# Performance work log

Hardware: AMD Instinct MI355X
Metric: run time of the kernel (lower is better)

Reference implementation:

```python
import jax, jax.numpy as jnp
import numpy as np
from jax import lax

CHAR_EMB = 30      # char_embedding_dim
N_FILT = 30        # num_cnn_filter (depthwise multiplier)
KSIZE = 3          # char_kernel_size
WORD_EMB = 100     # word_embedding_dim
MAX_WLEN = 40      # max_word_len
N_CHARS = 102      # characters.id + 2
VOCAB = 400002     # GloVe 400k + unk + pad


def setup_inputs() -> dict:
    key = jax.random.key(0)
    k1, k2, k3, k4, k5, k6 = jax.random.split(key, 6)
    B, S = 64, 128
    char_ids = jax.random.randint(k1, (B, S, MAX_WLEN), 0, N_CHARS)
    word_ids = jax.random.randint(k2, (B, S), 0, VOCAB)
    bound = (3.0 / CHAR_EMB) ** 0.5
    char_emb = jax.random.uniform(k3, (N_CHARS, CHAR_EMB), minval=-bound, maxval=bound, dtype=jnp.float32)
    # grouped Conv1d: out=CHAR_EMB*N_FILT=900, in_per_group=1, kernel=3 (OIH layout)
    fan = 1 * KSIZE + N_FILT * KSIZE
    xav = (6.0 / fan) ** 0.5
    conv_w = jax.random.uniform(k4, (CHAR_EMB * N_FILT, 1, KSIZE), minval=-xav, maxval=xav, dtype=jnp.float32)
    conv_b = jnp.zeros((CHAR_EMB * N_FILT,), dtype=jnp.float32)
    glove = jax.random.normal(k5, (VOCAB, WORD_EMB), dtype=jnp.float32)
    return {"char_ids": char_ids, "word_ids": word_ids, "char_emb": char_emb,
            "conv_w": conv_w, "conv_b": conv_b, "glove": glove}


def reference(char_ids, word_ids, char_emb, conv_w, conv_b, glove):
    B, S, W = char_ids.shape
    # char embedding lookup: [B,S,W,E] -> NCH layout [B*S, E, W]
    x = char_emb[char_ids]                       # [B,S,W,30]
    x = jnp.transpose(x, (0, 1, 3, 2)).reshape(B * S, CHAR_EMB, W)
    # depthwise (grouped) conv, groups=30, multiplier=30 -> 900 out channels, length W-K+1
    y = lax.conv_general_dilated(
        x, conv_w, window_strides=(1,), padding="VALID",
        dimension_numbers=("NCH", "OIH", "NCH"),
        feature_group_count=CHAR_EMB)            # [B*S, 900, 38]
    y = y + conv_b[None, :, None]
    pooled = jnp.max(y, axis=2).reshape(B, S, CHAR_EMB * N_FILT)  # max-over-time
    glove_e = glove[word_ids]                    # [B,S,100]
    return jnp.concatenate([pooled, glove_e], axis=2)  # [B,S,1000]
```

## Files before the change

### kernel.cpp

```cpp
#include <hip/hip_runtime.h>
#include <hip/hip_bf16.h>

#define CHAR_EMB 30
#define NFILT    30
#define WLEN     40
#define TOUT     38
#define OUTC     900
#define WORD_EMB 100
#define ROWP     44

__global__ __launch_bounds__(256) void encoder_kernel(
    const int*   __restrict__ char_ids,
    const int*   __restrict__ word_ids,
    const float* __restrict__ char_emb,
    const float* __restrict__ conv_w,
    const float* __restrict__ conv_b,
    const float* __restrict__ glove,
    float*       __restrict__ out,
    int BS)
{
    const int n   = blockIdx.x;
    const int tid = threadIdx.x;

    __shared__ float xs[CHAR_EMB * ROWP];
    __shared__ int   cid[WLEN];

    if (tid < WLEN) cid[tid] = char_ids[n * WLEN + tid];
    __syncthreads();

    for (int i = tid; i < WLEN * CHAR_EMB; i += 256) {
        const int t = i / CHAR_EMB;
        const int c = i - t * CHAR_EMB;
        xs[c * ROWP + t] = char_emb[cid[t] * CHAR_EMB + c];
    }
    __syncthreads();

    float* orow = out + (long)n * (OUTC + WORD_EMB);

    for (int o = tid; o < OUTC; o += 256) {
        const int g = o / NFILT;
        const float w0 = conv_w[o * 3 + 0];
        const float w1 = conv_w[o * 3 + 1];
        const float w2 = conv_w[o * 3 + 2];

        float xr[WLEN];
        const float4* rp = reinterpret_cast<const float4*>(&xs[g * ROWP]);
        #pragma unroll
        for (int k = 0; k < WLEN / 4; ++k) {
            float4 q = rp[k];
            xr[4 * k + 0] = q.x;
            xr[4 * k + 1] = q.y;
            xr[4 * k + 2] = q.z;
            xr[4 * k + 3] = q.w;
        }

        float m = -3.4e38f;
        #pragma unroll
        for (int t = 0; t < TOUT; ++t) {
            float v = fmaf(w0, xr[t], fmaf(w1, xr[t + 1], w2 * xr[t + 2]));
            m = fmaxf(m, v);
        }
        orow[o] = m + conv_b[o];
    }

    if (tid < WORD_EMB) {
        const int wid = word_ids[n];
        orow[OUTC + tid] = glove[(long)wid * WORD_EMB + tid];
    }
}

extern "C" void kernel_launch(void* const* d_in, const int* in_sizes, int n_in,
                              void* d_out, int out_size, void* d_ws, size_t ws_size,
                              hipStream_t stream) {
    const int*   char_ids = (const int*)  d_in[0];
    const int*   word_ids = (const int*)  d_in[1];
    const float* char_emb = (const float*)d_in[2];
    const float* conv_w   = (const float*)d_in[3];
    const float* conv_b   = (const float*)d_in[4];
    const float* glove    = (const float*)d_in[5];
    float*       out      = (float*)      d_out;

    const int BS = in_sizes[1];

    encoder_kernel<<<BS, 256, 0, stream>>>(
        char_ids, word_ids, char_emb, conv_w, conv_b, glove, out, BS);
}
```

Baseline: 235.1 us.

## Process two words per block with float2 interleaving and three filters per thread

Each block now handles two words: their char embeddings are interleaved as float2 in shared memory, and each of 300 threads computes three filters of one group over both words. The input row is loaded into registers once per thread and reused across the three filters and both words, so shared-memory reads and weight loads are amortised, and the grid is halved. The cost is more register pressure (a 40-element float2 array plus 9 weights), 20 idle threads per block, and more work per thread on a grid of half the size.

```diff
diff --git a/kernel.cpp b/kernel.cpp
--- a/kernel.cpp
+++ b/kernel.cpp
@@ -7,9 +7,19 @@
 #define TOUT     38
 #define OUTC     900
 #define WORD_EMB 100
-#define ROWP     44
+#define RP2      42
 
-__global__ __launch_bounds__(256) void encoder_kernel(
+__device__ __forceinline__ float2 f2fma(float w, float2 a, float2 c) {
+    return make_float2(fmaf(w, a.x, c.x), fmaf(w, a.y, c.y));
+}
+__device__ __forceinline__ float2 f2mul(float w, float2 a) {
+    return make_float2(w * a.x, w * a.y);
+}
+__device__ __forceinline__ float2 f2max(float2 a, float2 b) {
+    return make_float2(fmaxf(a.x, b.x), fmaxf(a.y, b.y));
+}
+
+__global__ __launch_bounds__(320) void encoder_kernel(
     const int*   __restrict__ char_ids,
     const int*   __restrict__ word_ids,
     const float* __restrict__ char_emb,
@@ -19,53 +29,71 @@
     float*       __restrict__ out,
     int BS)
 {
-    const int n   = blockIdx.x;
+    const int nA  = 2 * blockIdx.x;
+    const int nB  = nA + 1;
+    const bool hasB = (nB < BS);
     const int tid = threadIdx.x;
 
-    __shared__ float xs[CHAR_EMB * ROWP];
-    __shared__ int   cid[WLEN];
+    __shared__ __align__(16) float2 xs[CHAR_EMB * RP2];
+    __shared__ int cidA[WLEN];
+    __shared__ int cidB[WLEN];
 
-    if (tid < WLEN) cid[tid] = char_ids[n * WLEN + tid];
+    if (tid < WLEN)                    cidA[tid]        = char_ids[nA * WLEN + tid];
+    else if (tid < 2 * WLEN && hasB)   cidB[tid - WLEN] = char_ids[nB * WLEN + (tid - WLEN)];
+    else if (tid < 2 * WLEN)           cidB[tid - WLEN] = 0;
     __syncthreads();
 
-    for (int i = tid; i < WLEN * CHAR_EMB; i += 256) {
+    for (int i = tid; i < WLEN * CHAR_EMB; i += 320) {
         const int t = i / CHAR_EMB;
         const int c = i - t * CHAR_EMB;
-        xs[c * ROWP + t] = char_emb[cid[t] * CHAR_EMB + c];
+        const float a = char_emb[cidA[t] * CHAR_EMB + c];
+        const float b = char_emb[cidB[t] * CHAR_EMB + c];
+        xs[c * RP2 + t] = make_float2(a, b);
     }
     __syncthreads();
 
-    float* orow = out + (long)n * (OUTC + WORD_EMB);
+    float* orowA = out + (long)nA * (OUTC + WORD_EMB);
+    float* orowB = out + (long)nB * (OUTC + WORD_EMB);
 
-    for (int o = tid; o < OUTC; o += 256) {
-        const int g = o / NFILT;
-        const float w0 = conv_w[o * 3 + 0];
-        const float w1 = conv_w[o * 3 + 1];
-        const float w2 = conv_w[o * 3 + 2];
+    if (tid < 300) {
+        const int o0 = 3 * tid;
+        const int g  = tid / 10;
 
-        float xr[WLEN];
-        const float4* rp = reinterpret_cast<const float4*>(&xs[g * ROWP]);
+        float2 xr[WLEN];
+        const float4* rp = reinterpret_cast<const float4*>(&xs[g * RP2]);
         #pragma unroll
-        for (int k = 0; k < WLEN / 4; ++k) {
+        for (int k = 0; k < WLEN / 2; ++k) {
             float4 q = rp[k];
-            xr[4 * k + 0] = q.x;
-            xr[4 * k + 1] = q.y;
-            xr[4 * k + 2] = q.z;
-            xr[4 * k + 3] = q.w;
+            xr[2 * k + 0] = make_float2(q.x, q.y);
+            xr[2 * k + 1] = make_float2(q.z, q.w);
         }
 
-        float m = -3.4e38f;
+        float w[9];
         #pragma unroll
-        for (int t = 0; t < TOUT; ++t) {
-            float v = fmaf(w0, xr[t], fmaf(w1, xr[t + 1], w2 * xr[t + 2]));
-            m = fmaxf(m, v);
+        for (int j = 0; j < 9; ++j) w[j] = conv_w[9 * tid + j];
+
+        #pragma unroll
+        for (int f = 0; f < 3; ++f) {
+            const float w0 = w[3 * f + 0], w1 = w[3 * f + 1], w2 = w[3 * f + 2];
+            float2 m2 = make_float2(-3.4e38f, -3.4e38f);
+            #pragma unroll
+            for (int t = 0; t < TOUT; ++t) {
+                float2 v = f2fma(w0, xr[t], f2fma(w1, xr[t + 1], f2mul(w2, xr[t + 2])));
+                m2 = f2max(m2, v);
+            }
+            const float b = conv_b[o0 + f];
+            orowA[o0 + f] = m2.x + b;
+            if (hasB) orowB[o0 + f] = m2.y + b;
         }
-        orow[o] = m + conv_b[o];
     }
 
     if (tid < WORD_EMB) {
-        const int wid = word_ids[n];
-        orow[OUTC + tid] = glove[(long)wid * WORD_EMB + tid];
+        const int wid = word_ids[nA];
+        orowA[OUTC + tid] = glove[(long)wid * WORD_EMB + tid];
+    } else if (tid < 2 * WORD_EMB && hasB) {
+        const int j = tid - WORD_EMB;
+        const int wid = word_ids[nB];
+        orowB[OUTC + j] = glove[(long)wid * WORD_EMB + j];
     }
 }
 
@@ -81,7 +109,8 @@
     float*       out      = (float*)      d_out;
 
     const int BS = in_sizes[1];
+    const int nblk = (BS + 1) / 2;
 
-    encoder_kernel<<<BS, 256, 0, stream>>>(
+    encoder_kernel<<<nblk, 320, 0, stream>>>(
         char_ids, word_ids, char_emb, conv_w, conv_b, glove, out, BS);
 }
```

New measurement: 253.8 us. 8.0% more time.

## Process two words per block with interleaved float2 smem and per-group thread mapping

Applied to the files above, without the earlier changes.

Each block now handles two words. Their char embeddings are interleaved as float2 in shared memory so one row load serves both words, and the conv is computed with paired float2 FMAs. The thread mapping changes to 8 threads per group, each looping over filters, which reuses the loaded row across about 4 filters and removes the 900/256 tail imbalance. The glove copy moves to float4 and is issued before the barrier. In exchange, per-thread register pressure rises and the grid shrinks to half as many blocks.

```diff
diff --git a/kernel.cpp b/kernel.cpp
--- a/kernel.cpp
+++ b/kernel.cpp
@@ -7,7 +7,14 @@
 #define TOUT     38
 #define OUTC     900
 #define WORD_EMB 100
-#define ROWP     44
+#define RP2      42
+
+__device__ __forceinline__ float2 F2FMA(float2 w, float2 a, float2 c) {
+    return make_float2(fmaf(w.x, a.x, c.x), fmaf(w.y, a.y, c.y));
+}
+__device__ __forceinline__ float2 F2MUL(float2 w, float2 a) {
+    return make_float2(w.x * a.x, w.y * a.y);
+}
 
 __global__ __launch_bounds__(256) void encoder_kernel(
     const int*   __restrict__ char_ids,
@@ -19,53 +26,76 @@
     float*       __restrict__ out,
     int BS)
 {
-    const int n   = blockIdx.x;
-    const int tid = threadIdx.x;
+    const int nA   = 2 * blockIdx.x;
+    const int nB   = nA + 1;
+    const bool hasB = (nB < BS);
+    const int tid  = threadIdx.x;
 
-    __shared__ float xs[CHAR_EMB * ROWP];
-    __shared__ int   cid[WLEN];
+    __shared__ int cid[2 * WLEN];
+    __shared__ __align__(16) float2 xs[CHAR_EMB * RP2];
 
-    if (tid < WLEN) cid[tid] = char_ids[n * WLEN + tid];
+    float* orowA = out + (long)nA * (OUTC + WORD_EMB);
+    float* orowB = out + (long)nB * (OUTC + WORD_EMB);
+
+    if (tid < 25) {
+        const float4* gp = reinterpret_cast<const float4*>(glove + (long)word_ids[nA] * WORD_EMB);
+        reinterpret_cast<float4*>(orowA + OUTC)[tid] = gp[tid];
+    } else if (tid < 50 && hasB) {
+        const int j = tid - 25;
+        const float4* gp = reinterpret_cast<const float4*>(glove + (long)word_ids[nB] * WORD_EMB);
+        reinterpret_cast<float4*>(orowB + OUTC)[j] = gp[j];
+    }
+
+    if (tid < 2 * WLEN) {
+        cid[tid] = (tid < WLEN || hasB) ? char_ids[nA * WLEN + tid] : 0;
+    }
     __syncthreads();
 
     for (int i = tid; i < WLEN * CHAR_EMB; i += 256) {
         const int t = i / CHAR_EMB;
         const int c = i - t * CHAR_EMB;
-        xs[c * ROWP + t] = char_emb[cid[t] * CHAR_EMB + c];
+        const float a = char_emb[cid[t] * CHAR_EMB + c];
+        const float b = char_emb[cid[WLEN + t] * CHAR_EMB + c];
+        xs[c * RP2 + t] = make_float2(a, b);
     }
     __syncthreads();
 
-    float* orow = out + (long)n * (OUTC + WORD_EMB);
+    if (tid < 240) {
+        const int g = tid >> 3;
+        const int j = tid & 7;
 
-    for (int o = tid; o < OUTC; o += 256) {
-        const int g = o / NFILT;
-        const float w0 = conv_w[o * 3 + 0];
-        const float w1 = conv_w[o * 3 + 1];
-        const float w2 = conv_w[o * 3 + 2];
-
-        float xr[WLEN];
-        const float4* rp = reinterpret_cast<const float4*>(&xs[g * ROWP]);
+        float2 xr[WLEN];
+        const float4* rp = reinterpret_cast<const float4*>(&xs[g * RP2]);
         #pragma unroll
-        for (int k = 0; k < WLEN / 4; ++k) {
+        for (int k = 0; k < WLEN / 2; ++k) {
             float4 q = rp[k];
-            xr[4 * k + 0] = q.x;
-            xr[4 * k + 1] = q.y;
-            xr[4 * k + 2] = q.z;
-            xr[4 * k + 3] = q.w;
+            xr[2 * k + 0] = make_float2(q.x, q.y);
+            xr[2 * k + 1] = make_float2(q.z, q.w);
         }
 
-        float m = -3.4e38f;
         #pragma unroll
-        for (int t = 0; t < TOUT; ++t) {
-            float v = fmaf(w0, xr[t], fmaf(w1, xr[t + 1], w2 * xr[t + 2]));
-            m = fmaxf(m, v);
+        for (int f = j; f < NFILT; f += 8) {
+            const int o = g * NFILT + f;
+            const float w0 = conv_w[o * 3 + 0];
+            const float w1 = conv_w[o * 3 + 1];
+            const float w2 = conv_w[o * 3 + 2];
+            const float2 W0 = make_float2(w0, w0);
+            const float2 W1 = make_float2(w1, w1);
+            const float2 W2 = make_float2(w2, w2);
+
+            float mA = -3.4e38f, mB = -3.4e38f;
+            #pragma unroll
+            for (int i = 0; i < TOUT / 2; ++i) {
+                const int t = 2 * i;
+                float2 v0 = F2FMA(W0, xr[t],     F2FMA(W1, xr[t + 1], F2MUL(W2, xr[t + 2])));
+                float2 v1 = F2FMA(W0, xr[t + 1], F2FMA(W1, xr[t + 2], F2MUL(W2, xr[t + 3])));
+                mA = fmaxf(fmaxf(mA, v0.x), v1.x);
+                mB = fmaxf(fmaxf(mB, v0.y), v1.y);
+            }
+            const float b = conv_b[o];
+            orowA[o] = mA + b;
+            if (hasB) orowB[o] = mB + b;
         }
-        orow[o] = m + conv_b[o];
-    }
-
-    if (tid < WORD_EMB) {
-        const int wid = word_ids[n];
-        orow[OUTC + tid] = glove[(long)wid * WORD_EMB + tid];
     }
 }
 
@@ -81,7 +111,8 @@
     float*       out      = (float*)      d_out;
 
     const int BS = in_sizes[1];
+    const int nblk = (BS + 1) / 2;
 
-    encoder_kernel<<<BS, 256, 0, stream>>>(
+    encoder_kernel<<<nblk, 256, 0, stream>>>(
         char_ids, word_ids, char_emb, conv_w, conv_b, glove, out, BS);
 }
```

After: 234.9 us. Within noise of the previous version (-0.1%).
